# Performance work log

Measured on AMD Instinct MI355X. Metric: run time of the kernel, lower is better.

Reference implementation:

```python
import jax, jax.numpy as jnp
import numpy as np

B = 64
H = 1024          # hidden_size
C = 128           # C_out
L = 2             # num_layers
T_OUT = 256


def _uniform(key, shape, scale):
    return jax.random.uniform(key, shape, jnp.float32, -scale, scale)


def setup_inputs() -> dict:
    key = jax.random.key(0)
    ks = jax.random.split(key, 12)
    s = 1.0 / np.sqrt(H)  # torch RNN init scale
    return {
        "hidden":  jax.random.normal(ks[0], (L, B, H), jnp.float32),
        "frame_0": jax.random.normal(ks[1], (B, C, 1), jnp.float32),
        # GRU layer 0 (input_size = C)
        "W_ih0": _uniform(ks[2], (3 * H, C), s),
        "W_hh0": _uniform(ks[3], (3 * H, H), s),
        "b_ih0": _uniform(ks[4], (3 * H,), s),
        "b_hh0": _uniform(ks[5], (3 * H,), s),
        # GRU layer 1 (input_size = H)
        "W_ih1": _uniform(ks[6], (3 * H, H), s),
        "W_hh1": _uniform(ks[7], (3 * H, H), s),
        "b_ih1": _uniform(ks[8], (3 * H,), s),
        "b_hh1": _uniform(ks[9], (3 * H,), s),
        # output FC: hidden_size -> C_out
        "fc_W": _uniform(ks[10], (C, H), 1.0 / np.sqrt(H)),
        "fc_b": _uniform(ks[11], (C,), 1.0 / np.sqrt(H)),
    }


def _gru_cell(x, h, W_ih, W_hh, b_ih, b_hh):
    # torch gate order: r, z, n
    gi = x @ W_ih.T + b_ih            # (B, 3H)
    gh = h @ W_hh.T + b_hh            # (B, 3H)
    i_r, i_z, i_n = jnp.split(gi, 3, axis=-1)
    h_r, h_z, h_n = jnp.split(gh, 3, axis=-1)
    r = jax.nn.sigmoid(i_r + h_r)
    z = jax.nn.sigmoid(i_z + h_z)
    n = jnp.tanh(i_n + r * h_n)
    return (1.0 - z) * n + z * h


def reference(hidden, frame_0, W_ih0, W_hh0, b_ih0, b_hh0,
              W_ih1, W_hh1, b_ih1, b_hh1, fc_W, fc_b):
    x0 = frame_0[:, :, 0]  # permute(0,2,1) then seq len 1 -> (B, C)

    def step(carry, _):
        h, x = carry                        # h: (L,B,H), x: (B,C)
        h0 = _gru_cell(x,  h[0], W_ih0, W_hh0, b_ih0, b_hh0)
        h1 = _gru_cell(h0, h[1], W_ih1, W_hh1, b_ih1, b_hh1)
        y = h1 @ fc_W.T + fc_b              # (B, C), fed back as next input
        return (jnp.stack([h0, h1]), y), y

    (_, _), ys = jax.lax.scan(step, (hidden, x0), None, length=T_OUT)
    # ys: (T, B, C) -> cat along time (dim=1 in torch) then permute -> (B, C, T)
    return jnp.transpose(ys, (1, 2, 0))
```

## Files before the change

### kernel.cpp

```cpp
#include <hip/hip_runtime.h>
#include <hip/hip_bf16.h>


typedef __bf16 bf16_t;
typedef __bf16 bf8 __attribute__((ext_vector_type(8)));
typedef float  f4  __attribute__((ext_vector_type(4)));
typedef float  f2  __attribute__((ext_vector_type(2)));
typedef unsigned long long u64;
typedef u64 u64x2 __attribute__((ext_vector_type(2)));

static constexpr unsigned O_FLAGS = 0;
static constexpr unsigned O_FLG   = 1024;
static constexpr unsigned O_B0F   = 4096;
static constexpr unsigned O_X0    = O_B0F + 12288;
static constexpr unsigned O_H0B   = O_X0  + 16384;
static constexpr unsigned O_H1B   = O_H0B + 131072;
static constexpr unsigned O_GH0   = O_H1B + 262144;
static constexpr unsigned O_GH1   = O_GH0 + 786432;
static constexpr unsigned O_W0F   = O_GH1 + 786432;

#define LDS_EXTRA 98304
#define LDS_SIZE  131072

__device__ __forceinline__ void sfence() { __builtin_amdgcn_sched_barrier(0); }

__device__ __forceinline__ float sigmoidf_(float x) { return 1.f / (1.f + __expf(-x)); }
__device__ __forceinline__ float tanhf_(float x) {
  float e = __expf(-2.f * fabsf(x));
  float t = (1.f - e) / (1.f + e);
  return x < 0.f ? -t : t;
}

__device__ __forceinline__ u64 llc_ld64(const void* p) {
  return __hip_atomic_load((u64*)p, __ATOMIC_RELAXED, __HIP_MEMORY_SCOPE_AGENT);
}
__device__ __forceinline__ unsigned llc_ld32(const unsigned* p) {
  return __hip_atomic_load((unsigned*)p, __ATOMIC_RELAXED, __HIP_MEMORY_SCOPE_AGENT);
}
__device__ __forceinline__ void llc_st32(unsigned* p, unsigned v) {
  __hip_atomic_store(p, v, __ATOMIC_RELAXED, __HIP_MEMORY_SCOPE_AGENT);
}
__device__ __forceinline__ void llc_st2f(float* p, float x, float y) {
  f2 v = {x, y};
  __hip_atomic_store((u64*)p, __builtin_bit_cast(u64, v), __ATOMIC_RELAXED, __HIP_MEMORY_SCOPE_AGENT);
}
__device__ __forceinline__ f2 llc_ld2f(const float* p) {
  return __builtin_bit_cast(f2, llc_ld64(p));
}


template<int NKS, int RS>
__device__ __forceinline__ void gemm3(const bf16_t* __restrict__ Afm,
                                      const char* lds, int lane, int rt,
                                      f4& c0, f4& c1, f4& c2)
{
  const int lo = lane & 15, hi = lane >> 4;
  const bf16_t* ap = Afm + (size_t)rt * (NKS * 512) + lane * 8;
  const int sw = lo & 7;
  const char* l0 = lds + lo * RS;
  const char* l1 = lds + (16 + lo) * RS;
  const char* l2 = lds + (32 + lo) * RS;
  u64 a0[NKS], a1[NKS];
#pragma unroll
  for (int p = 0; p < NKS; ++p) {
    a0[p] = llc_ld64(ap + p * 512);
    a1[p] = llc_ld64(ap + p * 512 + 4);
  }
  int xo0 = (hi ^ sw) * 16;
  bf8 b0 = *(const bf8*)(l0 + xo0);
  bf8 b1 = *(const bf8*)(l1 + xo0);
  bf8 b2 = *(const bf8*)(l2 + xo0);
#pragma unroll
  for (int ks = 0; ks < NKS; ++ks) {
    bf8 nb0, nb1, nb2;
    if (ks + 1 < NKS) {
      const int nxo = (((ks + 1) * 4 + hi) ^ sw) * 16;
      nb0 = *(const bf8*)(l0 + nxo);
      nb1 = *(const bf8*)(l1 + nxo);
      nb2 = *(const bf8*)(l2 + nxo);
    }
    u64x2 tt; tt.x = a0[ks]; tt.y = a1[ks];
    bf8 a = __builtin_bit_cast(bf8, tt);
    c0 = __builtin_amdgcn_mfma_f32_16x16x32_bf16(a, b0, c0, 0, 0, 0);
    c1 = __builtin_amdgcn_mfma_f32_16x16x32_bf16(a, b1, c1, 0, 0, 0);
    c2 = __builtin_amdgcn_mfma_f32_16x16x32_bf16(a, b2, c2, 0, 0, 0);
    b0 = nb0; b1 = nb1; b2 = nb2;
  }
}

__device__ __forceinline__ f4 gemm1(const bf16_t* __restrict__ Afm,
                                    const char* lds, int lane, int rt)
{
  const int lo = lane & 15, hi = lane >> 4;
  const bf16_t* ap = Afm + (size_t)rt * 16384 + lane * 8;
  const int sw = lo & 7;
  const char* lb = lds + lo * 2048;
  f4 acc = {0.f, 0.f, 0.f, 0.f};
  u64 a0[32], a1[32];
#pragma unroll
  for (int p = 0; p < 32; ++p) {
    a0[p] = llc_ld64(ap + p * 512);
    a1[p] = llc_ld64(ap + p * 512 + 4);
  }
  bf8 b = *(const bf8*)(lb + (hi ^ sw) * 16);
#pragma unroll
  for (int ks = 0; ks < 32; ++ks) {
    bf8 nb;
    if (ks + 1 < 32) nb = *(const bf8*)(lb + ((((ks + 1) * 4 + hi) ^ sw) * 16));
    u64x2 tt; tt.x = a0[ks]; tt.y = a1[ks];
    bf8 a = __builtin_bit_cast(bf8, tt);
    acc = __builtin_amdgcn_mfma_f32_16x16x32_bf16(a, b, acc, 0, 0, 0);
    b = nb;
  }
  return acc;
}

__device__ __forceinline__ void gh_store_cm(f4 c0, f4 c1, f4 c2, float* __restrict__ dst,
                                            float br, float bz, float bn, int base)
{
  llc_st2f(dst + base,              c0[0] + br, c0[1] + br);
  llc_st2f(dst + base + 2,          c0[2] + br, c0[3] + br);
  llc_st2f(dst + 65536 + base,      c1[0] + bz, c1[1] + bz);
  llc_st2f(dst + 65536 + base + 2,  c1[2] + bz, c1[3] + bz);
  llc_st2f(dst + 131072 + base,     c2[0] + bn, c2[1] + bn);
  llc_st2f(dst + 131072 + base + 2, c2[2] + bn, c2[3] + bn);
}
__device__ __forceinline__ void gh_load_cm(const float* __restrict__ src, int base,
                                           f4& g0, f4& g1, f4& g2)
{
  f2 a = llc_ld2f(src + base),              b = llc_ld2f(src + base + 2);
  f2 c = llc_ld2f(src + 65536 + base),      d = llc_ld2f(src + 65536 + base + 2);
  f2 e = llc_ld2f(src + 131072 + base),     f = llc_ld2f(src + 131072 + base + 2);
  g0[0] = a[0]; g0[1] = a[1]; g0[2] = b[0]; g0[3] = b[1];
  g1[0] = c[0]; g1[1] = c[1]; g1[2] = d[0]; g1[3] = d[1];
  g2[0] = e[0]; g2[1] = e[1]; g2[2] = f[0]; g2[3] = f[1];
}

__device__ __forceinline__ void gru_apply(f4 c0, f4 c1, f4 c2, f4 g0, f4 g1, f4 g2,
                                          float br, float bz, float bn,
                                          float hreg[4], bf16_t* __restrict__ hb,
                                          int hoff, int lo)
{
#pragma unroll
  for (int q = 0; q < 4; ++q) {
    float r = sigmoidf_(c0[q] + br + g0[q]);
    float z = sigmoidf_(c1[q] + bz + g1[q]);
    float n = tanhf_  (c2[q] + bn + r * g2[q]);
    float hv = (1.f - z) * n + z * hreg[q];
    hreg[q] = hv;
    unsigned my = (unsigned)__builtin_bit_cast(unsigned short, (bf16_t)hv);
    unsigned ot = __shfl_xor(my, 1, 64);
    if ((lo & 1) == 0)
      llc_st32((unsigned*)(hb + hoff + q * 8), my | (ot << 16));
  }
}

__global__ void __launch_bounds__(256, 1)
rnn_persist(const float* __restrict__ hidden, const float* __restrict__ frame0,
            const float* __restrict__ Wih0, const float* __restrict__ Whh0,
            const float* __restrict__ bih0, const float* __restrict__ bhh0,
            const float* __restrict__ Wih1, const float* __restrict__ Whh1,
            const float* __restrict__ bih1, const float* __restrict__ bhh1,
            const float* __restrict__ fcW, const float* __restrict__ fcb,
            float* __restrict__ out, char* __restrict__ ws)
{
  extern __shared__ char smem[];
  const int tid = threadIdx.x;
  const int bid = blockIdx.x;
  const int gid = bid >> 6;
  const int lid = bid & 63;
  const int lane = tid & 63;
  const int wv = tid >> 6;
  const int lo = lane & 15, hi = lane >> 4;

  unsigned* flags = (unsigned*)(ws + O_FLAGS);
  unsigned* flgA0 = (unsigned*)(ws + O_FLG);
  unsigned* flgA3 = (unsigned*)(ws + O_FLG + 256);
  unsigned* flgB1 = (unsigned*)(ws + O_FLG + 512);
  unsigned* flgB2 = (unsigned*)(ws + O_FLG + 768);
  float*  b0f  = (float*)(ws + O_B0F);
  bf16_t* x0b  = (bf16_t*)(ws + O_X0);
  bf16_t* h0b  = (bf16_t*)(ws + O_H0B);
  bf16_t* h1b  = (bf16_t*)(ws + O_H1B);
  float*  gh0w = (float*)(ws + O_GH0);
  float*  gh1w = (float*)(ws + O_GH1);
  bf16_t* w0fb = (bf16_t*)(ws + O_W0F);

  auto signal_flag = [&](unsigned* arr, unsigned val) {
    sfence();
    asm volatile("s_waitcnt vmcnt(0)" ::: "memory");
    __syncthreads();
    if (tid == 0) llc_st32(&arr[lid], val);
  };
  auto wait1 = [&](unsigned* arr, unsigned g) {
    if (tid < 64) { while (!__all(llc_ld32(&arr[tid]) >= g)) {} }
    __syncthreads();
    sfence();
  };
  auto wait2 = [&](unsigned* a, unsigned ga, unsigned* b, unsigned gb) {
    if (tid < 64) {
      for (;;) {
        unsigned va = llc_ld32(&a[tid]);
        unsigned vb = llc_ld32(&b[tid]);
        if (__all(va >= ga && vb >= gb)) break;
      }
    }
    __syncthreads();
    sfence();
  };
  auto barrier_heavy = [&]() {
    __syncthreads();
    if (tid == 0)
      __hip_atomic_store(&flags[bid], 1u, __ATOMIC_RELEASE, __HIP_MEMORY_SCOPE_AGENT);
    if (tid < 64) {
      const u64* fp = (const u64*)(flags) + tid * 2;
      for (;;) {
        u64 a = llc_ld64(fp), b = llc_ld64(fp + 1);
        if ((unsigned)a && (unsigned)(a >> 32) && (unsigned)b && (unsigned)(b >> 32)) break;
        __builtin_amdgcn_s_sleep(1);
      }
    }
    __syncthreads();
    __builtin_amdgcn_fence(__ATOMIC_ACQUIRE, "agent");
    sfence();
  };

  const int col = lid * 16 + lo;
  const int hoff = (wv * 32 + (lid >> 1)) * 512
                 + ((((lid & 1) << 1) + (lo >> 3)) * 16 + hi * 4) * 8 + (lo & 7);
  const int ghbase = col * 64 + wv * 16 + hi * 4;
  float hreg[4];

  {
#pragma unroll
    for (int it = 0; it < 2; ++it) {
      int idx = bid * 512 + it * 256 + tid;
      float v = hidden[idx];
      int layer = idx >> 16, rc = idx & 65535;
      int row = rc >> 10, c = rc & 1023;
      int f = ((row >> 4) * 32 + (c >> 5)) * 512 + (((c >> 3) & 3) * 16 + (row & 15)) * 8 + (c & 7);
      if (layer == 0) h0b[f] = (bf16_t)v;
      else            h1b[65536 + f] = (bf16_t)v;
    }
    if (gid == 0 || gid == 2) {
#pragma unroll
      for (int q = 0; q < 4; ++q) {
        int row = wv * 16 + hi * 4 + q;
        hreg[q] = hidden[(gid == 0 ? 0 : 65536) + (size_t)row * 1024 + col];
      }
    }
    if (bid < 32) {
      int idx = bid * 256 + tid;
      int row = idx >> 7, c = idx & 127;
      int f = ((row >> 4) * 4 + (c >> 5)) * 512 + (((c >> 3) & 3) * 16 + (row & 15)) * 8 + (c & 7);
      x0b[f] = (bf16_t)frame0[idx];
    }

    float* wih  = (float*)smem;
    float* fcbl = wih + 1536;
    float* fcwt = fcbl + 128;
    const int jbase = bid * 12;
    for (int i = 0; i < 6; ++i) { int ii = tid + 256 * i; wih[ii] = Wih0[(size_t)jbase * 128 + ii]; }
    if (tid < 128) fcbl[tid] = fcb[tid];
    __syncthreads();
    if (tid < 12) {
      float s = bih0[jbase + tid];
      for (int c = 0; c < 128; ++c) s += wih[tid * 128 + c] * fcbl[c];
      b0f[jbase + tid] = s;
    }
    for (int kt = 0; kt < 16; ++kt) {
      __syncthreads();
      for (int i = 0; i < 32; ++i) {
        int ii = tid + 256 * i; int c = ii >> 6, x = ii & 63;
        fcwt[ii] = fcW[(size_t)c * 1024 + kt * 64 + x];
      }
      __syncthreads();
      int x = tid & 63, jg = tid >> 6;
      for (int jj = 0; jj < 3; ++jj) {
        int j = jg * 3 + jj;
        float s = 0.f;
#pragma unroll 16
        for (int c = 0; c < 128; ++c) s += wih[j * 128 + c] * fcwt[c * 64 + x];
        w0fb[(size_t)(jbase + j) * 1024 + kt * 64 + x] = (bf16_t)s;
      }
    }
  }
  barrier_heavy();

  float brM = 0.f, bzM = 0.f, bnM = 0.f, br0 = 0.f, bz0 = 0.f, bn0 = 0.f, fcbr = 0.f;
  if (gid == 0) {
    brM = b0f[col]; bzM = b0f[1024 + col]; bnM = b0f[2048 + col];
    br0 = bih0[col]; bz0 = bih0[1024 + col]; bn0 = bih0[2048 + col];
  } else if (gid == 1) {
    brM = bhh0[col]; bzM = bhh0[1024 + col]; bnM = bhh0[2048 + col];
    if (lid < 8) fcbr = fcb[col];
  } else if (gid == 2) {
    brM = bih1[col]; bzM = bih1[1024 + col]; bnM = bih1[2048 + col];
  } else {
    brM = bhh1[col]; bzM = bhh1[1024 + col]; bnM = bhh1[2048 + col];
  }

  {
    if (gid == 0) {
      for (int i = 0; i < 24; ++i) {
        int cc = tid + 256 * i;
        int w = cc >> 7, x = cc & 127;
        int g = w >> 4, r = w & 15;
        size_t grow = (size_t)g * 1024 + lid * 16 + r;
        bf8 v = *(const bf8*)(w0fb + grow * 1024 + x * 8);
        *(bf8*)(smem + w * 2048 + ((x ^ (w & 7)) * 16)) = v;
      }
      for (int i = 0; i < 3; ++i) {
        int cc = tid + 256 * i;
        int w = cc >> 4, x = cc & 15;
        int g = w >> 4, r = w & 15;
        size_t grow = (size_t)g * 1024 + lid * 16 + r;
        const float* src = Wih0 + grow * 128 + x * 8;
        bf8 v;
#pragma unroll
        for (int e = 0; e < 8; ++e) v[e] = (bf16_t)src[e];
        *(bf8*)(smem + LDS_EXTRA + w * 256 + ((x ^ (w & 7)) * 16)) = v;
      }
    } else {
      const float* Wsrc = (gid == 1) ? Whh0 : (gid == 2) ? Wih1 : Whh1;
      for (int i = 0; i < 24; ++i) {
        int cc = tid + 256 * i;
        int w = cc >> 7, x = cc & 127;
        int g = w >> 4, r = w & 15;
        size_t grow = (size_t)g * 1024 + lid * 16 + r;
        const float* src = Wsrc + grow * 1024 + x * 8;
        bf8 v;
#pragma unroll
        for (int e = 0; e < 8; ++e) v[e] = (bf16_t)src[e];
        *(bf8*)(smem + w * 2048 + ((x ^ (w & 7)) * 16)) = v;
      }
      if (gid == 1 && lid < 8) {
        for (int i = 0; i < 8; ++i) {
          int cc = tid + 256 * i;
          int w = cc >> 7, x = cc & 127;
          const float* src = fcW + (size_t)(lid * 16 + w) * 1024 + x * 8;
          bf8 v;
#pragma unroll
          for (int e = 0; e < 8; ++e) v[e] = (bf16_t)src[e];
          *(bf8*)(smem + LDS_EXTRA + w * 2048 + ((x ^ (w & 7)) * 16)) = v;
        }
      }
    }
    if (gid == 1) {
      __syncthreads();
      f4 c0 = {0.f,0.f,0.f,0.f}, c1 = {0.f,0.f,0.f,0.f}, c2 = {0.f,0.f,0.f,0.f};
      gemm3<32, 2048>(h0b, (const char*)smem, lane, wv, c0, c1, c2);
      gh_store_cm(c0, c1, c2, gh0w, brM, bzM, bnM, ghbase);
      signal_flag(flgB1, 1);
    }
  }

  for (int t = 0; t < 256; ++t) {
    const bf16_t* h1prev = h1b + ((t + 1) & 1) * 65536;

    if (gid == 0) {
      if (t == 0) wait1(flgB1, 1);
      else        wait2(flgB1, (unsigned)(t + 1), flgB2, (unsigned)t);
      f4 g0, g1, g2;
      gh_load_cm(gh0w, ghbase, g0, g1, g2);
      f4 c0 = {0.f,0.f,0.f,0.f}, c1 = {0.f,0.f,0.f,0.f}, c2 = {0.f,0.f,0.f,0.f};
      if (t == 0) {
        gemm3<4, 256>(x0b, (const char*)smem + LDS_EXTRA, lane, wv, c0, c1, c2);
        gru_apply(c0, c1, c2, g0, g1, g2, br0, bz0, bn0, hreg, h0b, hoff, lo);
      } else {
        gemm3<32, 2048>(h1prev, (const char*)smem, lane, wv, c0, c1, c2);
        gru_apply(c0, c1, c2, g0, g1, g2, brM, bzM, bnM, hreg, h0b, hoff, lo);
      }
      signal_flag(flgA0, (unsigned)(t + 1));
    } else if (gid == 3) {
      if (t > 0) wait1(flgB2, (unsigned)t);
      f4 c0 = {0.f,0.f,0.f,0.f}, c1 = {0.f,0.f,0.f,0.f}, c2 = {0.f,0.f,0.f,0.f};
      gemm3<32, 2048>(h1prev, (const char*)smem, lane, wv, c0, c1, c2);
      gh_store_cm(c0, c1, c2, gh1w, brM, bzM, bnM, ghbase);
      signal_flag(flgA3, (unsigned)(t + 1));
    } else if (gid == 1) {
      if (lid < 8 && t > 0) {
        wait1(flgB2, (unsigned)t);
        f4 y = gemm1(h1prev, (const char*)smem + LDS_EXTRA, lane, wv);
#pragma unroll
        for (int q = 0; q < 4; ++q) {
          int row = wv * 16 + hi * 4 + q;
          out[(size_t)row * 32768 + (size_t)col * 256 + (t - 1)] = y[q] + fcbr;
        }
      }
      wait1(flgA0, (unsigned)(t + 1));
      if (t < 255) {
        f4 c0 = {0.f,0.f,0.f,0.f}, c1 = {0.f,0.f,0.f,0.f}, c2 = {0.f,0.f,0.f,0.f};
        gemm3<32, 2048>(h0b, (const char*)smem, lane, wv, c0, c1, c2);
        gh_store_cm(c0, c1, c2, gh0w, brM, bzM, bnM, ghbase);
      }
      signal_flag(flgB1, (unsigned)(t + 2));
    } else {
      wait2(flgA0, (unsigned)(t + 1), flgA3, (unsigned)(t + 1));
      f4 g0, g1, g2;
      gh_load_cm(gh1w, ghbase, g0, g1, g2);
      f4 c0 = {0.f,0.f,0.f,0.f}, c1 = {0.f,0.f,0.f,0.f}, c2 = {0.f,0.f,0.f,0.f};
      gemm3<32, 2048>(h0b, (const char*)smem, lane, wv, c0, c1, c2);
      gru_apply(c0, c1, c2, g0, g1, g2, brM, bzM, bnM, hreg,
                h1b + (t & 1) * 65536, hoff, lo);
      signal_flag(flgB2, (unsigned)(t + 1));
    }
  }

  if (gid == 1 && lid < 8) {
    wait1(flgB2, 256u);
    const bf16_t* h1last = h1b + 65536;
    f4 y = gemm1(h1last, (const char*)smem + LDS_EXTRA, lane, wv);
#pragma unroll
    for (int q = 0; q < 4; ++q) {
      int row = wv * 16 + hi * 4 + q;
      out[(size_t)row * 32768 + (size_t)col * 256 + 255] = y[q] + fcbr;
    }
  }
}

extern "C" void kernel_launch(void* const* d_in, const int* in_sizes, int n_in,
                              void* d_out, int out_size, void* d_ws, size_t ws_size,
                              hipStream_t stream)
{
  const float* hidden = (const float*)d_in[0];
  const float* frame0 = (const float*)d_in[1];
  const float* Wih0 = (const float*)d_in[2];
  const float* Whh0 = (const float*)d_in[3];
  const float* bih0 = (const float*)d_in[4];
  const float* bhh0 = (const float*)d_in[5];
  const float* Wih1 = (const float*)d_in[6];
  const float* Whh1 = (const float*)d_in[7];
  const float* bih1 = (const float*)d_in[8];
  const float* bhh1 = (const float*)d_in[9];
  const float* fcW  = (const float*)d_in[10];
  const float* fcb  = (const float*)d_in[11];
  float* out = (float*)d_out;
  char*  ws  = (char*)d_ws;

  hipMemsetAsync(ws, 0, 4096, stream);

  hipFuncSetAttribute((const void*)rnn_persist,
                      hipFuncAttributeMaxDynamicSharedMemorySize, LDS_SIZE);

  void* args[] = { (void*)&hidden, (void*)&frame0, (void*)&Wih0, (void*)&Whh0,
                   (void*)&bih0, (void*)&bhh0, (void*)&Wih1, (void*)&Whh1,
                   (void*)&bih1, (void*)&bhh1, (void*)&fcW, (void*)&fcb,
                   (void*)&out, (void*)&ws };
  hipError_t err = hipLaunchCooperativeKernel((const void*)rnn_persist,
                                              dim3(256), dim3(256), args, LDS_SIZE, stream);
  if (err != hipSuccess) {
    rnn_persist<<<dim3(256), dim3(256), LDS_SIZE, stream>>>(
        hidden, frame0, Wih0, Whh0, bih0, bhh0, Wih1, Whh1, bih1, bhh1, fcW, fcb, out, ws);
  }
}
```

Baseline: 4.551 ms.

## Switch inter-block flags to per-wave granularity and store gate partials wave-contiguously

```diff
diff --git a/kernel.cpp b/kernel.cpp
--- a/kernel.cpp
+++ b/kernel.cpp
@@ -11,7 +11,7 @@
 
 static constexpr unsigned O_FLAGS = 0;
 static constexpr unsigned O_FLG   = 1024;
-static constexpr unsigned O_B0F   = 4096;
+static constexpr unsigned O_B0F   = 8192;
 static constexpr unsigned O_X0    = O_B0F + 12288;
 static constexpr unsigned O_H0B   = O_X0  + 16384;
 static constexpr unsigned O_H1B   = O_H0B + 131072;
@@ -40,12 +40,8 @@
 __device__ __forceinline__ void llc_st32(unsigned* p, unsigned v) {
   __hip_atomic_store(p, v, __ATOMIC_RELAXED, __HIP_MEMORY_SCOPE_AGENT);
 }
-__device__ __forceinline__ void llc_st2f(float* p, float x, float y) {
-  f2 v = {x, y};
-  __hip_atomic_store((u64*)p, __builtin_bit_cast(u64, v), __ATOMIC_RELAXED, __HIP_MEMORY_SCOPE_AGENT);
-}
-__device__ __forceinline__ f2 llc_ld2f(const float* p) {
-  return __builtin_bit_cast(f2, llc_ld64(p));
+__device__ __forceinline__ void llc_st64(u64* p, u64 v) {
+  __hip_atomic_store(p, v, __ATOMIC_RELAXED, __HIP_MEMORY_SCOPE_AGENT);
 }
 
 
@@ -115,22 +111,31 @@
   return acc;
 }
 
-__device__ __forceinline__ void gh_store_cm(f4 c0, f4 c1, f4 c2, float* __restrict__ dst,
-                                            float br, float bz, float bn, int base)
-{
-  llc_st2f(dst + base,              c0[0] + br, c0[1] + br);
-  llc_st2f(dst + base + 2,          c0[2] + br, c0[3] + br);
-  llc_st2f(dst + 65536 + base,      c1[0] + bz, c1[1] + bz);
-  llc_st2f(dst + 65536 + base + 2,  c1[2] + bz, c1[3] + bz);
-  llc_st2f(dst + 131072 + base,     c2[0] + bn, c2[1] + bn);
-  llc_st2f(dst + 131072 + base + 2, c2[2] + bn, c2[3] + bn);
-}
-__device__ __forceinline__ void gh_load_cm(const float* __restrict__ src, int base,
-                                           f4& g0, f4& g1, f4& g2)
-{
-  f2 a = llc_ld2f(src + base),              b = llc_ld2f(src + base + 2);
-  f2 c = llc_ld2f(src + 65536 + base),      d = llc_ld2f(src + 65536 + base + 2);
-  f2 e = llc_ld2f(src + 131072 + base),     f = llc_ld2f(src + 131072 + base + 2);
+__device__ __forceinline__ u64 pk2(float x, float y) {
+  f2 v = {x, y}; return __builtin_bit_cast(u64, v);
+}
+__device__ __forceinline__ void gh_store_soa(u64* g, int lid, int wv, int lane,
+                                             f4 c0, f4 c1, f4 c2,
+                                             float br, float bz, float bn)
+{
+  u64* p = g + ((size_t)lid * 24 + wv) * 64 + lane;
+  llc_st64(p,        pk2(c0[0] + br, c0[1] + br));
+  llc_st64(p + 256,  pk2(c0[2] + br, c0[3] + br));
+  llc_st64(p + 512,  pk2(c1[0] + bz, c1[1] + bz));
+  llc_st64(p + 768,  pk2(c1[2] + bz, c1[3] + bz));
+  llc_st64(p + 1024, pk2(c2[0] + bn, c2[1] + bn));
+  llc_st64(p + 1280, pk2(c2[2] + bn, c2[3] + bn));
+}
+__device__ __forceinline__ void gh_load_soa(const u64* g, int lid, int wv, int lane,
+                                            f4& g0, f4& g1, f4& g2)
+{
+  const u64* p = g + ((size_t)lid * 24 + wv) * 64 + lane;
+  f2 a = __builtin_bit_cast(f2, llc_ld64(p));
+  f2 b = __builtin_bit_cast(f2, llc_ld64(p + 256));
+  f2 c = __builtin_bit_cast(f2, llc_ld64(p + 512));
+  f2 d = __builtin_bit_cast(f2, llc_ld64(p + 768));
+  f2 e = __builtin_bit_cast(f2, llc_ld64(p + 1024));
+  f2 f = __builtin_bit_cast(f2, llc_ld64(p + 1280));
   g0[0] = a[0]; g0[1] = a[1]; g0[2] = b[0]; g0[3] = b[1];
   g1[0] = c[0]; g1[1] = c[1]; g1[2] = d[0]; g1[3] = d[1];
   g2[0] = e[0]; g2[1] = e[1]; g2[2] = f[0]; g2[3] = f[1];
@@ -175,37 +180,35 @@
 
   unsigned* flags = (unsigned*)(ws + O_FLAGS);
   unsigned* flgA0 = (unsigned*)(ws + O_FLG);
-  unsigned* flgA3 = (unsigned*)(ws + O_FLG + 256);
-  unsigned* flgB1 = (unsigned*)(ws + O_FLG + 512);
-  unsigned* flgB2 = (unsigned*)(ws + O_FLG + 768);
+  unsigned* flgA3 = (unsigned*)(ws + O_FLG + 1024);
+  unsigned* flgB1 = (unsigned*)(ws + O_FLG + 2048);
+  unsigned* flgB2 = (unsigned*)(ws + O_FLG + 3072);
   float*  b0f  = (float*)(ws + O_B0F);
   bf16_t* x0b  = (bf16_t*)(ws + O_X0);
   bf16_t* h0b  = (bf16_t*)(ws + O_H0B);
   bf16_t* h1b  = (bf16_t*)(ws + O_H1B);
-  float*  gh0w = (float*)(ws + O_GH0);
-  float*  gh1w = (float*)(ws + O_GH1);
+  u64*    gh0w = (u64*)(ws + O_GH0);
+  u64*    gh1w = (u64*)(ws + O_GH1);
   bf16_t* w0fb = (bf16_t*)(ws + O_W0F);
 
-  auto signal_flag = [&](unsigned* arr, unsigned val) {
+  auto signalw = [&](unsigned* arr, unsigned val) {
     sfence();
     asm volatile("s_waitcnt vmcnt(0)" ::: "memory");
-    __syncthreads();
-    if (tid == 0) llc_st32(&arr[lid], val);
+    if (lane == 0) llc_st32(&arr[wv * 64 + lid], val);
   };
-  auto wait1 = [&](unsigned* arr, unsigned g) {
-    if (tid < 64) { while (!__all(llc_ld32(&arr[tid]) >= g)) {} }
-    __syncthreads();
+  auto waitw1 = [&](const unsigned* arr, unsigned g) {
+    const unsigned* p = arr + wv * 64 + lane;
+    while (!__all(llc_ld32(p) >= g)) {}
     sfence();
   };
-  auto wait2 = [&](unsigned* a, unsigned ga, unsigned* b, unsigned gb) {
-    if (tid < 64) {
-      for (;;) {
-        unsigned va = llc_ld32(&a[tid]);
-        unsigned vb = llc_ld32(&b[tid]);
-        if (__all(va >= ga && vb >= gb)) break;
-      }
-    }
-    __syncthreads();
+  auto waitw2 = [&](const unsigned* a, unsigned ga, const unsigned* b, unsigned gb) {
+    const unsigned* pa = a + wv * 64 + lane;
+    const unsigned* pb = b + wv * 64 + lane;
+    for (;;) {
+      unsigned va = llc_ld32(pa);
+      unsigned vb = llc_ld32(pb);
+      if (__all(va >= ga && vb >= gb)) break;
+    }
     sfence();
   };
   auto barrier_heavy = [&]() {
@@ -228,7 +231,6 @@
   const int col = lid * 16 + lo;
   const int hoff = (wv * 32 + (lid >> 1)) * 512
                  + ((((lid & 1) << 1) + (lo >> 3)) * 16 + hi * 4) * 8 + (lo & 7);
-  const int ghbase = col * 64 + wv * 16 + hi * 4;
   float hreg[4];
 
   {
@@ -346,12 +348,12 @@
         }
       }
     }
+    __syncthreads();
     if (gid == 1) {
-      __syncthreads();
       f4 c0 = {0.f,0.f,0.f,0.f}, c1 = {0.f,0.f,0.f,0.f}, c2 = {0.f,0.f,0.f,0.f};
       gemm3<32, 2048>(h0b, (const char*)smem, lane, wv, c0, c1, c2);
-      gh_store_cm(c0, c1, c2, gh0w, brM, bzM, bnM, ghbase);
-      signal_flag(flgB1, 1);
+      gh_store_soa(gh0w, lid, wv, lane, c0, c1, c2, brM, bzM, bnM);
+      signalw(flgB1, 1);
     }
   }
 
@@ -359,10 +361,10 @@
     const bf16_t* h1prev = h1b + ((t + 1) & 1) * 65536;
 
     if (gid == 0) {
-      if (t == 0) wait1(flgB1, 1);
-      else        wait2(flgB1, (unsigned)(t + 1), flgB2, (unsigned)t);
+      if (t == 0) waitw1(flgB1, 1);
+      else        waitw2(flgB1, (unsigned)(t + 1), flgB2, (unsigned)t);
       f4 g0, g1, g2;
-      gh_load_cm(gh0w, ghbase, g0, g1, g2);
+      gh_load_soa(gh0w, lid, wv, lane, g0, g1, g2);
       f4 c0 = {0.f,0.f,0.f,0.f}, c1 = {0.f,0.f,0.f,0.f}, c2 = {0.f,0.f,0.f,0.f};
       if (t == 0) {
         gemm3<4, 256>(x0b, (const char*)smem + LDS_EXTRA, lane, wv, c0, c1, c2);
@@ -371,16 +373,21 @@
         gemm3<32, 2048>(h1prev, (const char*)smem, lane, wv, c0, c1, c2);
         gru_apply(c0, c1, c2, g0, g1, g2, brM, bzM, bnM, hreg, h0b, hoff, lo);
       }
-      signal_flag(flgA0, (unsigned)(t + 1));
+      signalw(flgA0, (unsigned)(t + 1));
     } else if (gid == 3) {
-      if (t > 0) wait1(flgB2, (unsigned)t);
+      if (t > 0) waitw1(flgB2, (unsigned)t);
       f4 c0 = {0.f,0.f,0.f,0.f}, c1 = {0.f,0.f,0.f,0.f}, c2 = {0.f,0.f,0.f,0.f};
       gemm3<32, 2048>(h1prev, (const char*)smem, lane, wv, c0, c1, c2);
-      gh_store_cm(c0, c1, c2, gh1w, brM, bzM, bnM, ghbase);
-      signal_flag(flgA3, (unsigned)(t + 1));
+      gh_store_soa(gh1w, lid, wv, lane, c0, c1, c2, brM, bzM, bnM);
+      signalw(flgA3, (unsigned)(t + 1));
     } else if (gid == 1) {
+      waitw1(flgA0, (unsigned)(t + 1));
+      if (t < 255) {
+        f4 c0 = {0.f,0.f,0.f,0.f}, c1 = {0.f,0.f,0.f,0.f}, c2 = {0.f,0.f,0.f,0.f};
+        gemm3<32, 2048>(h0b, (const char*)smem, lane, wv, c0, c1, c2);
+        gh_store_soa(gh0w, lid, wv, lane, c0, c1, c2, brM, bzM, bnM);
+      }
       if (lid < 8 && t > 0) {
-        wait1(flgB2, (unsigned)t);
         f4 y = gemm1(h1prev, (const char*)smem + LDS_EXTRA, lane, wv);
 #pragma unroll
         for (int q = 0; q < 4; ++q) {
@@ -388,27 +395,21 @@
           out[(size_t)row * 32768 + (size_t)col * 256 + (t - 1)] = y[q] + fcbr;
         }
       }
-      wait1(flgA0, (unsigned)(t + 1));
-      if (t < 255) {
-        f4 c0 = {0.f,0.f,0.f,0.f}, c1 = {0.f,0.f,0.f,0.f}, c2 = {0.f,0.f,0.f,0.f};
-        gemm3<32, 2048>(h0b, (const char*)smem, lane, wv, c0, c1, c2);
-        gh_store_cm(c0, c1, c2, gh0w, brM, bzM, bnM, ghbase);
-      }
-      signal_flag(flgB1, (unsigned)(t + 2));
+      signalw(flgB1, (unsigned)(t + 2));
     } else {
-      wait2(flgA0, (unsigned)(t + 1), flgA3, (unsigned)(t + 1));
+      waitw2(flgA0, (unsigned)(t + 1), flgA3, (unsigned)(t + 1));
       f4 g0, g1, g2;
-      gh_load_cm(gh1w, ghbase, g0, g1, g2);
+      gh_load_soa(gh1w, lid, wv, lane, g0, g1, g2);
       f4 c0 = {0.f,0.f,0.f,0.f}, c1 = {0.f,0.f,0.f,0.f}, c2 = {0.f,0.f,0.f,0.f};
       gemm3<32, 2048>(h0b, (const char*)smem, lane, wv, c0, c1, c2);
       gru_apply(c0, c1, c2, g0, g1, g2, brM, bzM, bnM, hreg,
                 h1b + (t & 1) * 65536, hoff, lo);
-      signal_flag(flgB2, (unsigned)(t + 1));
+      signalw(flgB2, (unsigned)(t + 1));
     }
   }
 
   if (gid == 1 && lid < 8) {
-    wait1(flgB2, 256u);
+    waitw1(flgB2, 256u);
     const bf16_t* h1last = h1b + 65536;
     f4 y = gemm1(h1last, (const char*)smem + LDS_EXTRA, lane, wv);
 #pragma unroll
@@ -438,7 +439,7 @@
   float* out = (float*)d_out;
   char*  ws  = (char*)d_ws;
 
-  hipMemsetAsync(ws, 0, 4096, stream);
+  hipMemsetAsync(ws, 0, 8192, stream);
 
   hipFuncSetAttribute((const void*)rnn_persist,
                       hipFuncAttributeMaxDynamicSharedMemorySize, LDS_SIZE);
```

New measurement: 5.234 ms. 15.0% more time.
